# Performance work log

Measured on AMD Instinct MI355X. Metric: run time of the kernel, lower is better.

Reference implementation:

```python
import jax, jax.numpy as jnp
import numpy as np

NUM_USERS = 100000
NUM_ITEMS = 50000
N_NODES = NUM_USERS + NUM_ITEMS
N_EDGES = 2_000_000
D = 64          # embedding_dim
HEADS = 4
F1 = D // HEADS  # per-head out dim of gat1
BATCH = 16384
NEG_SLOPE = 0.2  # PyG GATConv default negative_slope


def setup_inputs() -> dict:
    key = jax.random.key(0)
    ks = jax.random.split(key, 13)
    inp = {}
    inp["edge_index"] = jax.random.randint(ks[0], (2, N_EDGES), 0, N_NODES, dtype=jnp.int64)
    inp["batch_user_idx"] = jax.random.randint(ks[1], (BATCH,), 0, NUM_USERS, dtype=jnp.int64)
    inp["batch_item_idx"] = jax.random.randint(ks[2], (BATCH,), 0, NUM_ITEMS, dtype=jnp.int64)
    # Embedding tables (nn.init.normal_ std=0.01)
    inp["user_emb"] = 0.01 * jax.random.normal(ks[3], (NUM_USERS, D), dtype=jnp.float32)
    inp["item_emb"] = 0.01 * jax.random.normal(ks[4], (NUM_ITEMS, D), dtype=jnp.float32)
    # gat1: GATConv(64, 16, heads=4, concat=True)
    inp["W1"] = jax.random.normal(ks[5], (D, HEADS * F1), dtype=jnp.float32) / np.sqrt(D)
    inp["a_src1"] = jax.random.normal(ks[6], (HEADS, F1), dtype=jnp.float32) / np.sqrt(F1)
    inp["a_dst1"] = jax.random.normal(ks[7], (HEADS, F1), dtype=jnp.float32) / np.sqrt(F1)
    inp["b1"] = jnp.zeros((HEADS * F1,), dtype=jnp.float32)
    # gat2: GATConv(64, 64, heads=1)
    inp["W2"] = jax.random.normal(ks[8], (D, D), dtype=jnp.float32) / np.sqrt(D)
    inp["a_src2"] = jax.random.normal(ks[9], (1, D), dtype=jnp.float32) / np.sqrt(D)
    inp["a_dst2"] = jax.random.normal(ks[10], (1, D), dtype=jnp.float32) / np.sqrt(D)
    inp["b2"] = jnp.zeros((D,), dtype=jnp.float32)
    return inp


def _gat_conv(x, src, dst, W, a_src, a_dst, b, num_nodes):
    """PyG GATConv (eval mode, concat, self-loops already in src/dst)."""
    H, F = a_src.shape
    h = (x @ W).reshape(num_nodes, H, F)                 # [N,H,F]
    alpha_s = jnp.einsum('nhf,hf->nh', h, a_src)         # [N,H]
    alpha_d = jnp.einsum('nhf,hf->nh', h, a_dst)
    e = alpha_s[src] + alpha_d[dst]                      # [E,H]
    e = jax.nn.leaky_relu(e, NEG_SLOPE)
    # scatter-softmax over destination neighborhoods
    m = jax.ops.segment_max(e, dst, num_segments=num_nodes)   # [N,H]
    e = jnp.exp(e - m[dst])
    denom = jax.ops.segment_sum(e, dst, num_segments=num_nodes)
    alpha = e / denom[dst]                               # [E,H]
    msg = h[src] * alpha[:, :, None]                     # [E,H,F]
    agg = jax.ops.segment_sum(msg, dst, num_segments=num_nodes)  # [N,H,F]
    return agg.reshape(num_nodes, H * F) + b


def reference(user_emb, item_emb, W1, a_src1, a_dst1, b1,
              W2, a_src2, a_dst2, b2,
              edge_index, batch_user_idx, batch_item_idx):
    x = jnp.concatenate([user_emb, item_emb], axis=0)    # [N,D]
    n = x.shape[0]
    loop = jnp.arange(n, dtype=edge_index.dtype)          # add_self_loops=True
    src = jnp.concatenate([edge_index[0], loop])
    dst = jnp.concatenate([edge_index[1], loop])
    x = jax.nn.elu(_gat_conv(x, src, dst, W1, a_src1, a_dst1, b1, n))
    x = jax.nn.elu(_gat_conv(x, src, dst, W2, a_src2, a_dst2, b2, n))
    u = x[batch_user_idx]
    v = x[batch_item_idx + NUM_USERS]
    return jax.nn.sigmoid(jnp.sum(u * v, axis=1))        # [BATCH]
```

## Files before the change

kernel.cpp:

```cpp
#include <hip/hip_runtime.h>
#include <math.h>

#define SHIFT 8
#define NBMAX 1024
#define CAP   4096
#define TILE  8192
#define HSCALE 64.0f

typedef float v2f __attribute__((ext_vector_type(2)));
typedef short bf16x8 __attribute__((ext_vector_type(8)));
typedef float f32x4 __attribute__((ext_vector_type(4)));

__device__ __forceinline__ unsigned short f2bf(float f) {
    unsigned u = __float_as_uint(f);
    unsigned r = u + 0x7FFFu + ((u >> 16) & 1u);
    return (unsigned short)(r >> 16);
}
__device__ __forceinline__ unsigned pack2bf(float lo, float hi) {
    return (unsigned)f2bf(lo) | ((unsigned)f2bf(hi) << 16);
}
__device__ __forceinline__ float bflo(unsigned u) { return __uint_as_float(u << 16); }
__device__ __forceinline__ float bfhi(unsigned u) { return __uint_as_float(u & 0xFFFF0000u); }


__global__ void k_prep_w(const float* __restrict__ W1, const float* __restrict__ W2,
                         unsigned short* __restrict__ WT1, unsigned short* __restrict__ WT2,
                         unsigned* __restrict__ gcur, int NB) {
    int t = blockIdx.x * 256 + threadIdx.x;
    if (t < 4096) {
        int n = t & 63, k = t >> 6;
        WT1[n * 64 + k] = f2bf(W1[k * 64 + n]);
        WT2[n * 64 + k] = f2bf(W2[k * 64 + n]);
    }
    if (t < NB) gcur[t] = (unsigned)t * CAP;
}


__global__ __launch_bounds__(512) void k_partition(
    const int* __restrict__ src, const int* __restrict__ dst, int E,
    unsigned* __restrict__ gcur, unsigned* __restrict__ pairs, int NB) {
    __shared__ unsigned lh[NBMAX];
    __shared__ unsigned lcur[NBMAX];
    int t = threadIdx.x;
    for (int q = t; q < NB; q += 512) lh[q] = 0;
    __syncthreads();
    int base = blockIdx.x * TILE;
    int end = min(E, base + TILE);
    for (int i = base + t; i < end; i += 512)
        atomicAdd(&lh[((unsigned)dst[i]) >> SHIFT], 1u);
    __syncthreads();
    for (int q = t; q < NB; q += 512) {
        unsigned c = lh[q];
        lcur[q] = c ? atomicAdd(&gcur[q], c) : 0u;
    }
    __syncthreads();
    for (int i = base + t; i < end; i += 512) {
        unsigned d = (unsigned)dst[i];
        unsigned pos = atomicAdd(&lcur[d >> SHIFT], 1u);
        pairs[pos] = ((d & 255u) << 18) | (unsigned)src[i];
    }
}

__global__ __launch_bounds__(512) void k_bucket_sort(
    const unsigned* __restrict__ pairs, const unsigned* __restrict__ gcur,
    unsigned* __restrict__ beg, unsigned* __restrict__ endd,
    int* __restrict__ srt, int N, int NB) {
    __shared__ unsigned lh[256];
    __shared__ unsigned lcur[256];
    __shared__ unsigned sh[256];
    __shared__ int ssrt[CAP];
    int b = blockIdx.x;
    int t = threadIdx.x;
    unsigned s0 = (unsigned)b * CAP;
    int cnt = (int)(gcur[b] - s0);
    if (t < 256) lh[t] = 0;
    __syncthreads();
    for (int i = t; i < cnt; i += 512)
        atomicAdd(&lh[pairs[s0 + i] >> 18], 1u);
    __syncthreads();
    unsigned deg_t = 0;
    if (t < 256) { deg_t = lh[t]; sh[t] = deg_t; }
    __syncthreads();
    for (int off = 1; off < 256; off <<= 1) {
        unsigned x = 0;
        if (t < 256 && t >= off) x = sh[t - off];
        __syncthreads();
        if (t < 256) sh[t] += x;
        __syncthreads();
    }
    if (t < 256) {
        unsigned excl = sh[t] - deg_t;
        lcur[t] = excl;
        int node = (b << SHIFT) + t;
        if (node < N) { beg[node] = s0 + excl; endd[node] = s0 + excl + deg_t; }
    }
    __syncthreads();
    for (int i = t; i < cnt; i += 512) {
        unsigned pk = pairs[s0 + i];
        unsigned p = atomicAdd(&lcur[pk >> 18], 1u);
        ssrt[p] = (int)(pk & 0x3FFFFu);
    }
    __syncthreads();
    for (int i = t; i < cnt; i += 512) srt[s0 + i] = ssrt[i];
}


template <int HT, int BIN>
__global__ __launch_bounds__(256) void k_linear_mfma(
    const void* __restrict__ xav, const void* __restrict__ xbv, int split,
    const unsigned short* __restrict__ WTg,
    const float* __restrict__ a_src, const float* __restrict__ a_dst,
    unsigned char* __restrict__ h, float* __restrict__ as_out,
    float* __restrict__ ad_out, int N) {
    __shared__ unsigned short sX[64 * 72];
    __shared__ unsigned short sWT[64 * 72];
    __shared__ float sH[64 * 68];
    int t = threadIdx.x;
    int nodeBase = blockIdx.x * 64;

    {
        int r = t >> 2, c4 = (t & 3) * 16;
        int n = nodeBase + r;
        uint4 A = {0,0,0,0}, Bv = {0,0,0,0};
        if (BIN) {
            if (n < N) {
                const unsigned short* row = (const unsigned short*)xav + (size_t)n * 64 + c4;
                A  = ((const uint4*)(const void*)row)[0];
                Bv = ((const uint4*)(const void*)row)[1];
            }
        } else {
            float4 v0 = {0,0,0,0}, v1 = {0,0,0,0}, v2 = {0,0,0,0}, v3 = {0,0,0,0};
            if (n < N) {
                const float* row = (n < split) ? ((const float*)xav + (size_t)n * 64 + c4)
                                               : ((const float*)xbv + (size_t)(n - split) * 64 + c4);
                const float4* r4 = (const float4*)row;
                v0 = r4[0]; v1 = r4[1]; v2 = r4[2]; v3 = r4[3];
            }
            A  = make_uint4(pack2bf(v0.x, v0.y), pack2bf(v0.z, v0.w),
                            pack2bf(v1.x, v1.y), pack2bf(v1.z, v1.w));
            Bv = make_uint4(pack2bf(v2.x, v2.y), pack2bf(v2.z, v2.w),
                            pack2bf(v3.x, v3.y), pack2bf(v3.z, v3.w));
        }
        *(uint4*)(void*)(sX + r * 72 + c4) = A;
        *(uint4*)(void*)(sX + r * 72 + c4 + 8) = Bv;
        const uint4* wsrc = (const uint4*)(const void*)WTg;
        int base = (r * 64 + c4) >> 3;
        *(uint4*)(void*)(sWT + r * 72 + c4) = wsrc[base];
        *(uint4*)(void*)(sWT + r * 72 + c4 + 8) = wsrc[base + 1];
    }
    __syncthreads();

    {
        int lane = t & 63, w = t >> 6;
        int gl = lane & 15, quad = lane >> 4;
        int m0 = w * 16;
        const bf16x8 a0 = *(const bf16x8*)(void*)(sX + (m0 + gl) * 72 + quad * 8);
        const bf16x8 a1 = *(const bf16x8*)(void*)(sX + (m0 + gl) * 72 + 32 + quad * 8);
        f32x4 acc[4];
#pragma unroll
        for (int tt = 0; tt < 4; ++tt) {
            const bf16x8 b0 = *(const bf16x8*)(void*)(sWT + (tt * 16 + gl) * 72 + quad * 8);
            const bf16x8 b1 = *(const bf16x8*)(void*)(sWT + (tt * 16 + gl) * 72 + 32 + quad * 8);
            f32x4 c = {0.f, 0.f, 0.f, 0.f};
            c = __builtin_amdgcn_mfma_f32_16x16x32_bf16(a0, b0, c, 0, 0, 0);
            c = __builtin_amdgcn_mfma_f32_16x16x32_bf16(a1, b1, c, 0, 0, 0);
            acc[tt] = c;
        }
#pragma unroll
        for (int tt = 0; tt < 4; ++tt)
#pragma unroll
            for (int rr = 0; rr < 4; ++rr)
                sH[(m0 + quad * 4 + rr) * 68 + tt * 16 + gl] = acc[tt][rr];
    }
    __syncthreads();

    {
        int m = t >> 2, p = t & 3;
        int n = nodeBase + m;
        const float4* sp = (const float4*)(void*)(sH + m * 68 + p * 16);
        float4 q0 = sp[0], q1 = sp[1], q2 = sp[2], q3 = sp[3];
        float hv[16] = {q0.x,q0.y,q0.z,q0.w, q1.x,q1.y,q1.z,q1.w,
                        q2.x,q2.y,q2.z,q2.w, q3.x,q3.y,q3.z,q3.w};
        if (n < N) {
            unsigned dwords[4];
#pragma unroll
            for (int q = 0; q < 4; ++q) {
                int d0 = __builtin_amdgcn_cvt_pk_fp8_f32(hv[4*q] * HSCALE, hv[4*q+1] * HSCALE, 0, false);
                d0 = __builtin_amdgcn_cvt_pk_fp8_f32(hv[4*q+2] * HSCALE, hv[4*q+3] * HSCALE, d0, true);
                dwords[q] = (unsigned)d0;
            }
            ((uint4*)h)[(size_t)n * 4 + p] = make_uint4(dwords[0], dwords[1], dwords[2], dwords[3]);
            float ps = 0.f, pd = 0.f;
#pragma unroll
            for (int i = 0; i < 16; ++i) {
                ps = fmaf(hv[i], a_src[p * 16 + i], ps);
                pd = fmaf(hv[i], a_dst[p * 16 + i], pd);
            }
            if (HT == 4) {
                as_out[n * 4 + p] = ps;
                ad_out[n * 4 + p] = pd;
            } else {
                ps += __shfl_xor(ps, 1, 64); ps += __shfl_xor(ps, 2, 64);
                pd += __shfl_xor(pd, 1, 64); pd += __shfl_xor(pd, 2, 64);
                if (p == 0) { as_out[n] = ps; ad_out[n] = pd; }
            }
        }
    }
}

template <int HT>
__global__ __launch_bounds__(256, 4) void k_gat(
                      const int* __restrict__ srt, const unsigned* __restrict__ beg,
                      const unsigned* __restrict__ endd,
                      const unsigned* __restrict__ hq, const float* __restrict__ as,
                      const float* __restrict__ ad, const float* __restrict__ b,
                      unsigned* __restrict__ xout, int N) {
    __shared__ unsigned s_vo[4][4][40];
    __shared__ float    s_w[4][4][(HT == 4) ? 164 : 40];

    int t = threadIdx.x;
    int lane = t & 63;
    int wv = t >> 6;
    int gl = lane & 15;
    int g  = lane >> 4;
    int wid = (int)((blockIdx.x * blockDim.x + t) >> 6);
    int d = wid * 4 + g;
    bool active = d < N;
    const int hh = (HT == 4) ? (gl >> 2) : 0;
    const unsigned gl4 = (unsigned)gl << 2;
    const char* hqb = (const char*)hq;
    const char* asb = (const char*)as;

    float adv = 0.f, l = 0.f;
    float a0 = 0.f, a1 = 0.f, a2 = 0.f, a3 = 0.f;
    int kb = 0, end = 0;
    if (active) {
        adv = ad[d * HT + hh];
        float e0 = as[d * HT + hh] + adv;
        e0 = (e0 > 0.f) ? e0 : 0.2f * e0;
        float w0 = __expf(e0);
        unsigned dw = hq[(size_t)d * 16 + gl];
        v2f lo = __builtin_amdgcn_cvt_pk_f32_fp8((int)dw, false);
        v2f hi = __builtin_amdgcn_cvt_pk_f32_fp8((int)dw, true);
        l = w0;
        a0 = w0 * lo.x; a1 = w0 * lo.y; a2 = w0 * hi.x; a3 = w0 * hi.y;
        kb = (int)beg[d];
        end = (int)endd[d];
    }

    int m = end - kb;
    while (__ballot(m > 0)) {
        unsigned v0 = 0, v1 = 0;
        if (gl < m)      v0 = ((unsigned)srt[kb + gl]) << 6;
        if (gl + 16 < m) v1 = ((unsigned)srt[kb + gl + 16]) << 6;

        if (HT == 1) {
            float as0 = 0.f, as1 = 0.f;
            if (gl < m)      as0 = *(const float*)(asb + (v0 >> 4));
            if (gl + 16 < m) as1 = *(const float*)(asb + (v1 >> 4));
            s_vo[wv][g][gl]      = v0;
            s_vo[wv][g][gl + 16] = v1;
            asm volatile("s_waitcnt lgkmcnt(0)" ::: "memory");
            __builtin_amdgcn_sched_barrier(0);
            unsigned rr[32];
            const uint4* vob = (const uint4*)(const void*)&s_vo[wv][g][0];
#pragma unroll
            for (int c = 0; c < 8; ++c) {
                uint4 vv = vob[c];
                rr[4*c+0] = *(const unsigned*)(hqb + (vv.x + gl4));
                rr[4*c+1] = *(const unsigned*)(hqb + (vv.y + gl4));
                rr[4*c+2] = *(const unsigned*)(hqb + (vv.z + gl4));
                rr[4*c+3] = *(const unsigned*)(hqb + (vv.w + gl4));
            }
            float w0 = 0.f, w1 = 0.f;
            if (gl < m) {
                float e = as0 + adv;
                e = (e > 0.f) ? e : 0.2f * e;
                w0 = __expf(e);
            }
            if (gl + 16 < m) {
                float e = as1 + adv;
                e = (e > 0.f) ? e : 0.2f * e;
                w1 = __expf(e);
            }
            float wsum = w0 + w1;
            wsum += __shfl_xor(wsum, 1, 64);
            wsum += __shfl_xor(wsum, 2, 64);
            wsum += __shfl_xor(wsum, 4, 64);
            wsum += __shfl_xor(wsum, 8, 64);
            l += wsum;
            s_w[wv][g][gl]      = w0;
            s_w[wv][g][gl + 16] = w1;
            asm volatile("s_waitcnt lgkmcnt(0)" ::: "memory");
            __builtin_amdgcn_sched_barrier(0);
            const float4* wrd = (const float4*)(const void*)&s_w[wv][g][0];
#pragma unroll
            for (int c = 0; c < 8; ++c) {
                float4 wc = wrd[c];
                float wj[4] = {wc.x, wc.y, wc.z, wc.w};
#pragma unroll
                for (int j = 0; j < 4; ++j) {
                    float w = wj[j];
                    unsigned rv = rr[4*c + j];
                    v2f lo = __builtin_amdgcn_cvt_pk_f32_fp8((int)rv, false);
                    v2f hi = __builtin_amdgcn_cvt_pk_f32_fp8((int)rv, true);
                    a0 = fmaf(w, lo.x, a0);
                    a1 = fmaf(w, lo.y, a1);
                    a2 = fmaf(w, hi.x, a2);
                    a3 = fmaf(w, hi.y, a3);
                }
            }
        } else {
            s_vo[wv][g][gl]      = v0;
            s_vo[wv][g][gl + 16] = v1;
            asm volatile("s_waitcnt lgkmcnt(0)" ::: "memory");
            __builtin_amdgcn_sched_barrier(0);
            int eb = (gl & 3) << 3;
            const uint4* vop = (const uint4*)(const void*)&s_vo[wv][g][eb];
            uint4 va = vop[0], vb = vop[1];
            unsigned vs[8] = {va.x, va.y, va.z, va.w, vb.x, vb.y, vb.z, vb.w};
            float av[8];
#pragma unroll
            for (int r = 0; r < 8; ++r)
                av[r] = *(const float*)(asb + ((vs[r] >> 2) + ((unsigned)hh << 2)));
            unsigned rr[32];
            const uint4* vob = (const uint4*)(const void*)&s_vo[wv][g][0];
#pragma unroll
            for (int c = 0; c < 8; ++c) {
                uint4 vv = vob[c];
                rr[4*c+0] = *(const unsigned*)(hqb + (vv.x + gl4));
                rr[4*c+1] = *(const unsigned*)(hqb + (vv.y + gl4));
                rr[4*c+2] = *(const unsigned*)(hqb + (vv.z + gl4));
                rr[4*c+3] = *(const unsigned*)(hqb + (vv.w + gl4));
            }
            float wq[8];
#pragma unroll
            for (int r = 0; r < 8; ++r) {
                wq[r] = 0.f;
                if (eb + r < m) {
                    float e = av[r] + adv;
                    e = (e > 0.f) ? e : 0.2f * e;
                    wq[r] = __expf(e);
                }
            }
            float wsum = ((wq[0] + wq[1]) + (wq[2] + wq[3]))
                       + ((wq[4] + wq[5]) + (wq[6] + wq[7]));
            wsum += __shfl_xor(wsum, 1, 64);
            wsum += __shfl_xor(wsum, 2, 64);
            l += wsum;
            float4* wp = (float4*)(void*)&s_w[wv][g][hh * 40 + eb];
            wp[0] = make_float4(wq[0], wq[1], wq[2], wq[3]);
            wp[1] = make_float4(wq[4], wq[5], wq[6], wq[7]);
            asm volatile("s_waitcnt lgkmcnt(0)" ::: "memory");
            __builtin_amdgcn_sched_barrier(0);
            const float4* wrd = (const float4*)(const void*)&s_w[wv][g][hh * 40];
#pragma unroll
            for (int c = 0; c < 8; ++c) {
                float4 wc = wrd[c];
                float wj[4] = {wc.x, wc.y, wc.z, wc.w};
#pragma unroll
                for (int j = 0; j < 4; ++j) {
                    float w = wj[j];
                    unsigned rv = rr[4*c + j];
                    v2f lo = __builtin_amdgcn_cvt_pk_f32_fp8((int)rv, false);
                    v2f hi = __builtin_amdgcn_cvt_pk_f32_fp8((int)rv, true);
                    a0 = fmaf(w, lo.x, a0);
                    a1 = fmaf(w, lo.y, a1);
                    a2 = fmaf(w, hi.x, a2);
                    a3 = fmaf(w, hi.y, a3);
                }
            }
        }
        kb += 32;
        m = end - kb;
    }

    if (active) {
        float4 bb4 = ((const float4*)b)[gl];
        float rs = 1.f / (l * HSCALE);
        float v0 = a0 * rs + bb4.x;
        float v1 = a1 * rs + bb4.y;
        float v2 = a2 * rs + bb4.z;
        float v3 = a3 * rs + bb4.w;
        float o0 = (v0 > 0.f) ? v0 : expm1f(v0);
        float o1 = (v1 > 0.f) ? v1 : expm1f(v1);
        float o2 = (v2 > 0.f) ? v2 : expm1f(v2);
        float o3 = (v3 > 0.f) ? v3 : expm1f(v3);
        ((uint2*)xout)[(size_t)d * 16 + gl] = make_uint2(pack2bf(o0, o1), pack2bf(o2, o3));
    }
}

__global__ void k_dot_sig(const uint2* __restrict__ x2, const int* __restrict__ uidx,
                          const int* __restrict__ vidx, float* __restrict__ out,
                          int batch, int numUsers) {
    int lane = threadIdx.x & 63;
    int gl = lane & 15;
    int q = (int)(((blockIdx.x * blockDim.x + threadIdx.x) >> 6) * 4 + (lane >> 4));
    if (q >= batch) return;
    int u = uidx[q];
    int v = vidx[q] + numUsers;
    uint2 a = x2[(size_t)u * 16 + gl];
    uint2 c = x2[(size_t)v * 16 + gl];
    float p = bflo(a.x) * bflo(c.x) + bfhi(a.x) * bfhi(c.x)
            + bflo(a.y) * bflo(c.y) + bfhi(a.y) * bfhi(c.y);
#pragma unroll
    for (int off = 1; off < 16; off <<= 1) p += __shfl_xor(p, off, 64);
    if (gl == 0) out[q] = 1.f / (1.f + __expf(-p));
}


static inline int cdiv(long long a, long long b) { return (int)((a + b - 1) / b); }

extern "C" void kernel_launch(void* const* d_in, const int* in_sizes, int n_in,
                              void* d_out, int out_size, void* d_ws, size_t ws_size,
                              hipStream_t stream) {
    const int* edge_index = (const int*)d_in[0];
    const int* buidx      = (const int*)d_in[1];
    const int* biidx      = (const int*)d_in[2];
    const float* user_emb = (const float*)d_in[3];
    const float* item_emb = (const float*)d_in[4];
    const float* W1     = (const float*)d_in[5];
    const float* a_src1 = (const float*)d_in[6];
    const float* a_dst1 = (const float*)d_in[7];
    const float* b1     = (const float*)d_in[8];
    const float* W2     = (const float*)d_in[9];
    const float* a_src2 = (const float*)d_in[10];
    const float* a_dst2 = (const float*)d_in[11];
    const float* b2     = (const float*)d_in[12];
    float* out = (float*)d_out;

    const int E  = in_sizes[0] / 2;
    const int B  = in_sizes[1];
    const int NU = in_sizes[3] / 64;
    const int NI = in_sizes[4] / 64;
    const int N  = NU + NI;
    const int NB = cdiv(N, 1 << SHIFT);

    const int* src = edge_index;
    const int* dst = edge_index + E;

    float* ws = (float*)d_ws;
    size_t off = 0;
    unsigned* x_buf  = (unsigned*)(ws + off); off += (size_t)N * 32;
    unsigned* h_buf  = (unsigned*)(ws + off); off += (size_t)N * 16;
    float*    as_b   = ws + off; off += (size_t)N * 4;
    float*    ad_b   = ws + off; off += (size_t)N * 4;
    unsigned* gcur_b = (unsigned*)(ws + off); off += NBMAX;
    unsigned* beg_b  = (unsigned*)(ws + off); off += (size_t)N;
    unsigned* end_b  = (unsigned*)(ws + off); off += (size_t)N;
    unsigned* pairs_b= (unsigned*)(ws + off); off += (size_t)NB * CAP;
    int*      srt_b  = (int*)(ws + off); off += (size_t)NB * CAP;
    unsigned short* wt1_b = (unsigned short*)(ws + off); off += 2048;
    unsigned short* wt2_b = (unsigned short*)(ws + off); off += 2048;

    const int BS = 256;

    k_prep_w<<<16, BS, 0, stream>>>(W1, W2, wt1_b, wt2_b, gcur_b, NB);
    k_partition<<<cdiv(E, TILE), 512, 0, stream>>>(src, dst, E, gcur_b, pairs_b, NB);
    k_bucket_sort<<<NB, 512, 0, stream>>>(pairs_b, gcur_b, beg_b, end_b, srt_b, N, NB);

    k_linear_mfma<4, 0><<<cdiv(N, 64), BS, 0, stream>>>(user_emb, item_emb, NU, wt1_b,
                                                        a_src1, a_dst1,
                                                        (unsigned char*)h_buf, as_b, ad_b, N);
    k_gat<4><<<cdiv((long long)N * 16, BS), BS, 0, stream>>>(
        srt_b, beg_b, end_b, h_buf, as_b, ad_b, b1, x_buf, N);

    k_linear_mfma<1, 1><<<cdiv(N, 64), BS, 0, stream>>>(x_buf, x_buf, N, wt2_b,
                                                        a_src2, a_dst2,
                                                        (unsigned char*)h_buf, as_b, ad_b, N);
    k_gat<1><<<cdiv((long long)N * 16, BS), BS, 0, stream>>>(
        srt_b, beg_b, end_b, h_buf, as_b, ad_b, b2, x_buf, N);

    k_dot_sig<<<cdiv((long long)B * 16, BS), BS, 0, stream>>>(
        (const uint2*)x_buf, buidx, biidx, out, B, NU);
}
```

Baseline: 250.9 us.

## Skip second half of gather chunk when wave degrees small; fold weight prep into partition

The GAT aggregation loop now takes the maximum remaining degree across each wave's four destinations and skips the second 16-neighbor half of each 32-edge chunk (index loads, feature gathers, FMAs) when no destination needs it. Accumulators switch to packed float2 vectors so the compiler can emit packed FMA instructions. The k_prep_w kernel is removed: weight transposition moves into k_partition, and the bucket cursor init becomes a memset with bucket offsets added inside partition. This trims one launch and wasted work for low-degree nodes (average degree is about 14), at the cost of extra shuffles and branches per iteration.

```diff
diff --git a/kernel.cpp b/kernel.cpp
--- a/kernel.cpp
+++ b/kernel.cpp
@@ -23,25 +23,22 @@
 __device__ __forceinline__ float bfhi(unsigned u) { return __uint_as_float(u & 0xFFFF0000u); }
 
 
-__global__ void k_prep_w(const float* __restrict__ W1, const float* __restrict__ W2,
-                         unsigned short* __restrict__ WT1, unsigned short* __restrict__ WT2,
-                         unsigned* __restrict__ gcur, int NB) {
-    int t = blockIdx.x * 256 + threadIdx.x;
-    if (t < 4096) {
-        int n = t & 63, k = t >> 6;
-        WT1[n * 64 + k] = f2bf(W1[k * 64 + n]);
-        WT2[n * 64 + k] = f2bf(W2[k * 64 + n]);
-    }
-    if (t < NB) gcur[t] = (unsigned)t * CAP;
-}
-
-
 __global__ __launch_bounds__(512) void k_partition(
     const int* __restrict__ src, const int* __restrict__ dst, int E,
-    unsigned* __restrict__ gcur, unsigned* __restrict__ pairs, int NB) {
+    unsigned* __restrict__ gcur, unsigned* __restrict__ pairs, int NB,
+    const float* __restrict__ W1, const float* __restrict__ W2,
+    unsigned short* __restrict__ WT1, unsigned short* __restrict__ WT2) {
     __shared__ unsigned lh[NBMAX];
     __shared__ unsigned lcur[NBMAX];
     int t = threadIdx.x;
+    {
+        int gt = blockIdx.x * 512 + t;
+        if (gt < 4096) {
+            int n = gt & 63, k = gt >> 6;
+            WT1[n * 64 + k] = f2bf(W1[k * 64 + n]);
+            WT2[n * 64 + k] = f2bf(W2[k * 64 + n]);
+        }
+    }
     for (int q = t; q < NB; q += 512) lh[q] = 0;
     __syncthreads();
     int base = blockIdx.x * TILE;
@@ -51,7 +48,7 @@
     __syncthreads();
     for (int q = t; q < NB; q += 512) {
         unsigned c = lh[q];
-        lcur[q] = c ? atomicAdd(&gcur[q], c) : 0u;
+        lcur[q] = c ? ((unsigned)q * CAP + atomicAdd(&gcur[q], c)) : 0u;
     }
     __syncthreads();
     for (int i = base + t; i < end; i += 512) {
@@ -72,7 +69,7 @@
     int b = blockIdx.x;
     int t = threadIdx.x;
     unsigned s0 = (unsigned)b * CAP;
-    int cnt = (int)(gcur[b] - s0);
+    int cnt = (int)gcur[b];
     if (t < 256) lh[t] = 0;
     __syncthreads();
     for (int i = t; i < cnt; i += 512)
@@ -232,7 +229,7 @@
     const char* asb = (const char*)as;
 
     float adv = 0.f, l = 0.f;
-    float a0 = 0.f, a1 = 0.f, a2 = 0.f, a3 = 0.f;
+    v2f acc01 = {0.f, 0.f}, acc23 = {0.f, 0.f};
     int kb = 0, end = 0;
     if (active) {
         adv = ad[d * HT + hh];
@@ -243,42 +240,58 @@
         v2f lo = __builtin_amdgcn_cvt_pk_f32_fp8((int)dw, false);
         v2f hi = __builtin_amdgcn_cvt_pk_f32_fp8((int)dw, true);
         l = w0;
-        a0 = w0 * lo.x; a1 = w0 * lo.y; a2 = w0 * hi.x; a3 = w0 * hi.y;
+        v2f wv2 = {w0, w0};
+        acc01 = wv2 * lo;
+        acc23 = wv2 * hi;
         kb = (int)beg[d];
         end = (int)endd[d];
     }
 
     int m = end - kb;
     while (__ballot(m > 0)) {
+        int mm = max(m, __shfl_xor(m, 16, 64));
+        mm = max(mm, __shfl_xor(mm, 32, 64));
+        const bool up = mm > 16;
+
         unsigned v0 = 0, v1 = 0;
-        if (gl < m)      v0 = ((unsigned)srt[kb + gl]) << 6;
-        if (gl + 16 < m) v1 = ((unsigned)srt[kb + gl + 16]) << 6;
+        if (gl < m)            v0 = ((unsigned)srt[kb + gl]) << 6;
+        if (up && gl + 16 < m) v1 = ((unsigned)srt[kb + gl + 16]) << 6;
 
         if (HT == 1) {
             float as0 = 0.f, as1 = 0.f;
-            if (gl < m)      as0 = *(const float*)(asb + (v0 >> 4));
-            if (gl + 16 < m) as1 = *(const float*)(asb + (v1 >> 4));
-            s_vo[wv][g][gl]      = v0;
-            s_vo[wv][g][gl + 16] = v1;
+            if (gl < m)            as0 = *(const float*)(asb + (v0 >> 4));
+            if (up && gl + 16 < m) as1 = *(const float*)(asb + (v1 >> 4));
+            s_vo[wv][g][gl] = v0;
+            if (up) s_vo[wv][g][gl + 16] = v1;
             asm volatile("s_waitcnt lgkmcnt(0)" ::: "memory");
             __builtin_amdgcn_sched_barrier(0);
             unsigned rr[32];
             const uint4* vob = (const uint4*)(const void*)&s_vo[wv][g][0];
 #pragma unroll
-            for (int c = 0; c < 8; ++c) {
+            for (int c = 0; c < 4; ++c) {
                 uint4 vv = vob[c];
                 rr[4*c+0] = *(const unsigned*)(hqb + (vv.x + gl4));
                 rr[4*c+1] = *(const unsigned*)(hqb + (vv.y + gl4));
                 rr[4*c+2] = *(const unsigned*)(hqb + (vv.z + gl4));
                 rr[4*c+3] = *(const unsigned*)(hqb + (vv.w + gl4));
             }
+            if (up) {
+#pragma unroll
+                for (int c = 4; c < 8; ++c) {
+                    uint4 vv = vob[c];
+                    rr[4*c+0] = *(const unsigned*)(hqb + (vv.x + gl4));
+                    rr[4*c+1] = *(const unsigned*)(hqb + (vv.y + gl4));
+                    rr[4*c+2] = *(const unsigned*)(hqb + (vv.z + gl4));
+                    rr[4*c+3] = *(const unsigned*)(hqb + (vv.w + gl4));
+                }
+            }
             float w0 = 0.f, w1 = 0.f;
             if (gl < m) {
                 float e = as0 + adv;
                 e = (e > 0.f) ? e : 0.2f * e;
                 w0 = __expf(e);
             }
-            if (gl + 16 < m) {
+            if (up && gl + 16 < m) {
                 float e = as1 + adv;
                 e = (e > 0.f) ? e : 0.2f * e;
                 w1 = __expf(e);
@@ -289,13 +302,13 @@
             wsum += __shfl_xor(wsum, 4, 64);
             wsum += __shfl_xor(wsum, 8, 64);
             l += wsum;
-            s_w[wv][g][gl]      = w0;
-            s_w[wv][g][gl + 16] = w1;
+            s_w[wv][g][gl] = w0;
+            if (up) s_w[wv][g][gl + 16] = w1;
             asm volatile("s_waitcnt lgkmcnt(0)" ::: "memory");
             __builtin_amdgcn_sched_barrier(0);
             const float4* wrd = (const float4*)(const void*)&s_w[wv][g][0];
 #pragma unroll
-            for (int c = 0; c < 8; ++c) {
+            for (int c = 0; c < 4; ++c) {
                 float4 wc = wrd[c];
                 float wj[4] = {wc.x, wc.y, wc.z, wc.w};
 #pragma unroll
@@ -304,15 +317,31 @@
                     unsigned rv = rr[4*c + j];
                     v2f lo = __builtin_amdgcn_cvt_pk_f32_fp8((int)rv, false);
                     v2f hi = __builtin_amdgcn_cvt_pk_f32_fp8((int)rv, true);
-                    a0 = fmaf(w, lo.x, a0);
-                    a1 = fmaf(w, lo.y, a1);
-                    a2 = fmaf(w, hi.x, a2);
-                    a3 = fmaf(w, hi.y, a3);
+                    v2f wv2 = {w, w};
+                    acc01 += wv2 * lo;
+                    acc23 += wv2 * hi;
+                }
+            }
+            if (up) {
+#pragma unroll
+                for (int c = 4; c < 8; ++c) {
+                    float4 wc = wrd[c];
+                    float wj[4] = {wc.x, wc.y, wc.z, wc.w};
+#pragma unroll
+                    for (int j = 0; j < 4; ++j) {
+                        float w = wj[j];
+                        unsigned rv = rr[4*c + j];
+                        v2f lo = __builtin_amdgcn_cvt_pk_f32_fp8((int)rv, false);
+                        v2f hi = __builtin_amdgcn_cvt_pk_f32_fp8((int)rv, true);
+                        v2f wv2 = {w, w};
+                        acc01 += wv2 * lo;
+                        acc23 += wv2 * hi;
+                    }
                 }
             }
         } else {
             s_vo[wv][g][gl]      = v0;
-            s_vo[wv][g][gl + 16] = v1;
+            s_vo[wv][g][gl + 16] = (up && gl + 16 < m) ? v1 : 0u;
             asm volatile("s_waitcnt lgkmcnt(0)" ::: "memory");
             __builtin_amdgcn_sched_barrier(0);
             int eb = (gl & 3) << 3;
@@ -326,12 +355,22 @@
             unsigned rr[32];
             const uint4* vob = (const uint4*)(const void*)&s_vo[wv][g][0];
 #pragma unroll
-            for (int c = 0; c < 8; ++c) {
+            for (int c = 0; c < 4; ++c) {
                 uint4 vv = vob[c];
                 rr[4*c+0] = *(const unsigned*)(hqb + (vv.x + gl4));
                 rr[4*c+1] = *(const unsigned*)(hqb + (vv.y + gl4));
                 rr[4*c+2] = *(const unsigned*)(hqb + (vv.z + gl4));
                 rr[4*c+3] = *(const unsigned*)(hqb + (vv.w + gl4));
+            }
+            if (up) {
+#pragma unroll
+                for (int c = 4; c < 8; ++c) {
+                    uint4 vv = vob[c];
+                    rr[4*c+0] = *(const unsigned*)(hqb + (vv.x + gl4));
+                    rr[4*c+1] = *(const unsigned*)(hqb + (vv.y + gl4));
+                    rr[4*c+2] = *(const unsigned*)(hqb + (vv.z + gl4));
+                    rr[4*c+3] = *(const unsigned*)(hqb + (vv.w + gl4));
+                }
             }
             float wq[8];
 #pragma unroll
@@ -355,7 +394,7 @@
             __builtin_amdgcn_sched_barrier(0);
             const float4* wrd = (const float4*)(const void*)&s_w[wv][g][hh * 40];
 #pragma unroll
-            for (int c = 0; c < 8; ++c) {
+            for (int c = 0; c < 4; ++c) {
                 float4 wc = wrd[c];
                 float wj[4] = {wc.x, wc.y, wc.z, wc.w};
 #pragma unroll
@@ -364,10 +403,26 @@
                     unsigned rv = rr[4*c + j];
                     v2f lo = __builtin_amdgcn_cvt_pk_f32_fp8((int)rv, false);
                     v2f hi = __builtin_amdgcn_cvt_pk_f32_fp8((int)rv, true);
-                    a0 = fmaf(w, lo.x, a0);
-                    a1 = fmaf(w, lo.y, a1);
-                    a2 = fmaf(w, hi.x, a2);
-                    a3 = fmaf(w, hi.y, a3);
+                    v2f wv2 = {w, w};
+                    acc01 += wv2 * lo;
+                    acc23 += wv2 * hi;
+                }
+            }
+            if (up) {
+#pragma unroll
+                for (int c = 4; c < 8; ++c) {
+                    float4 wc = wrd[c];
+                    float wj[4] = {wc.x, wc.y, wc.z, wc.w};
+#pragma unroll
+                    for (int j = 0; j < 4; ++j) {
+                        float w = wj[j];
+                        unsigned rv = rr[4*c + j];
+                        v2f lo = __builtin_amdgcn_cvt_pk_f32_fp8((int)rv, false);
+                        v2f hi = __builtin_amdgcn_cvt_pk_f32_fp8((int)rv, true);
+                        v2f wv2 = {w, w};
+                        acc01 += wv2 * lo;
+                        acc23 += wv2 * hi;
+                    }
                 }
             }
         }
@@ -378,10 +433,10 @@
     if (active) {
         float4 bb4 = ((const float4*)b)[gl];
         float rs = 1.f / (l * HSCALE);
-        float v0 = a0 * rs + bb4.x;
-        float v1 = a1 * rs + bb4.y;
-        float v2 = a2 * rs + bb4.z;
-        float v3 = a3 * rs + bb4.w;
+        float v0 = acc01.x * rs + bb4.x;
+        float v1 = acc01.y * rs + bb4.y;
+        float v2 = acc23.x * rs + bb4.z;
+        float v3 = acc23.y * rs + bb4.w;
         float o0 = (v0 > 0.f) ? v0 : expm1f(v0);
         float o1 = (v1 > 0.f) ? v1 : expm1f(v1);
         float o2 = (v2 > 0.f) ? v2 : expm1f(v2);
@@ -455,8 +510,9 @@
 
     const int BS = 256;
 
-    k_prep_w<<<16, BS, 0, stream>>>(W1, W2, wt1_b, wt2_b, gcur_b, NB);
-    k_partition<<<cdiv(E, TILE), 512, 0, stream>>>(src, dst, E, gcur_b, pairs_b, NB);
+    hipMemsetAsync(gcur_b, 0, NBMAX * sizeof(unsigned), stream);
+    k_partition<<<cdiv(E, TILE), 512, 0, stream>>>(src, dst, E, gcur_b, pairs_b, NB,
+                                                   W1, W2, wt1_b, wt2_b);
     k_bucket_sort<<<NB, 512, 0, stream>>>(pairs_b, gcur_b, beg_b, end_b, srt_b, N, NB);
 
     k_linear_mfma<4, 0><<<cdiv(N, 64), BS, 0, stream>>>(user_emb, item_emb, NU, wt1_b,
```

Measured after the change: 252.6 us. About the same (+0.7%).

## Merge bucket sort and first linear layer into one launch; fold weight prep into partition

Applied to the files above, without the earlier changes.

Weight transposition to bf16 moves into the partition kernel, and the per-bucket cursor init becomes a memset, with offsets now relative to each bucket base. The bucket sort and the layer-1 MFMA linear transform become one kernel: the first NB blocks sort and the rest compute h, sharing LDS through a union. The aim is to remove launch overhead and let two independent stages run concurrently on the GPU. The cost is that the linear blocks now use 512 threads with half of them idle in the MFMA and epilogue phases, and the union raises LDS per block to the larger of the two layouts.

```diff
diff --git a/kernel.cpp b/kernel.cpp
--- a/kernel.cpp
+++ b/kernel.cpp
@@ -23,25 +23,22 @@
 __device__ __forceinline__ float bfhi(unsigned u) { return __uint_as_float(u & 0xFFFF0000u); }
 
 
-__global__ void k_prep_w(const float* __restrict__ W1, const float* __restrict__ W2,
-                         unsigned short* __restrict__ WT1, unsigned short* __restrict__ WT2,
-                         unsigned* __restrict__ gcur, int NB) {
-    int t = blockIdx.x * 256 + threadIdx.x;
-    if (t < 4096) {
-        int n = t & 63, k = t >> 6;
-        WT1[n * 64 + k] = f2bf(W1[k * 64 + n]);
-        WT2[n * 64 + k] = f2bf(W2[k * 64 + n]);
-    }
-    if (t < NB) gcur[t] = (unsigned)t * CAP;
-}
-
-
 __global__ __launch_bounds__(512) void k_partition(
     const int* __restrict__ src, const int* __restrict__ dst, int E,
-    unsigned* __restrict__ gcur, unsigned* __restrict__ pairs, int NB) {
+    unsigned* __restrict__ gcur, unsigned* __restrict__ pairs, int NB,
+    const float* __restrict__ W1, const float* __restrict__ W2,
+    unsigned short* __restrict__ WT1, unsigned short* __restrict__ WT2) {
     __shared__ unsigned lh[NBMAX];
     __shared__ unsigned lcur[NBMAX];
     int t = threadIdx.x;
+    {
+        int gt = blockIdx.x * 512 + t;
+        if (gt < 4096) {
+            int n = gt & 63, k = gt >> 6;
+            WT1[n * 64 + k] = f2bf(W1[k * 64 + n]);
+            WT2[n * 64 + k] = f2bf(W2[k * 64 + n]);
+        }
+    }
     for (int q = t; q < NB; q += 512) lh[q] = 0;
     __syncthreads();
     int base = blockIdx.x * TILE;
@@ -51,7 +48,7 @@
     __syncthreads();
     for (int q = t; q < NB; q += 512) {
         unsigned c = lh[q];
-        lcur[q] = c ? atomicAdd(&gcur[q], c) : 0u;
+        lcur[q] = c ? ((unsigned)q * CAP + atomicAdd(&gcur[q], c)) : 0u;
     }
     __syncthreads();
     for (int i = base + t; i < end; i += 512) {
@@ -61,47 +58,125 @@
     }
 }
 
-__global__ __launch_bounds__(512) void k_bucket_sort(
+__global__ __launch_bounds__(512) void k_buck_lin(
     const unsigned* __restrict__ pairs, const unsigned* __restrict__ gcur,
     unsigned* __restrict__ beg, unsigned* __restrict__ endd,
-    int* __restrict__ srt, int N, int NB) {
-    __shared__ unsigned lh[256];
-    __shared__ unsigned lcur[256];
-    __shared__ unsigned sh[256];
-    __shared__ int ssrt[CAP];
-    int b = blockIdx.x;
+    int* __restrict__ srt, int N, int NB,
+    const float* __restrict__ xa, const float* __restrict__ xb, int split,
+    const unsigned short* __restrict__ WTg,
+    const float* __restrict__ a_src, const float* __restrict__ a_dst,
+    unsigned char* __restrict__ h, float* __restrict__ as_out,
+    float* __restrict__ ad_out) {
+    __shared__ union U {
+        struct { unsigned lh[256]; unsigned lcur[256]; unsigned sh[256]; int ssrt[CAP]; } b;
+        struct { unsigned short sX[64 * 72]; unsigned short sWT[64 * 72]; float sH[64 * 68]; } l;
+    } u;
     int t = threadIdx.x;
-    unsigned s0 = (unsigned)b * CAP;
-    int cnt = (int)(gcur[b] - s0);
-    if (t < 256) lh[t] = 0;
-    __syncthreads();
-    for (int i = t; i < cnt; i += 512)
-        atomicAdd(&lh[pairs[s0 + i] >> 18], 1u);
-    __syncthreads();
-    unsigned deg_t = 0;
-    if (t < 256) { deg_t = lh[t]; sh[t] = deg_t; }
-    __syncthreads();
-    for (int off = 1; off < 256; off <<= 1) {
-        unsigned x = 0;
-        if (t < 256 && t >= off) x = sh[t - off];
-        __syncthreads();
-        if (t < 256) sh[t] += x;
-        __syncthreads();
-    }
-    if (t < 256) {
-        unsigned excl = sh[t] - deg_t;
-        lcur[t] = excl;
-        int node = (b << SHIFT) + t;
-        if (node < N) { beg[node] = s0 + excl; endd[node] = s0 + excl + deg_t; }
-    }
-    __syncthreads();
-    for (int i = t; i < cnt; i += 512) {
-        unsigned pk = pairs[s0 + i];
-        unsigned p = atomicAdd(&lcur[pk >> 18], 1u);
-        ssrt[p] = (int)(pk & 0x3FFFFu);
-    }
-    __syncthreads();
-    for (int i = t; i < cnt; i += 512) srt[s0 + i] = ssrt[i];
+
+    if ((int)blockIdx.x < NB) {
+        int b = blockIdx.x;
+        unsigned s0 = (unsigned)b * CAP;
+        int cnt = (int)gcur[b];
+        if (t < 256) u.b.lh[t] = 0;
+        __syncthreads();
+        for (int i = t; i < cnt; i += 512)
+            atomicAdd(&u.b.lh[pairs[s0 + i] >> 18], 1u);
+        __syncthreads();
+        unsigned deg_t = 0;
+        if (t < 256) { deg_t = u.b.lh[t]; u.b.sh[t] = deg_t; }
+        __syncthreads();
+        for (int off = 1; off < 256; off <<= 1) {
+            unsigned x = 0;
+            if (t < 256 && t >= off) x = u.b.sh[t - off];
+            __syncthreads();
+            if (t < 256) u.b.sh[t] += x;
+            __syncthreads();
+        }
+        if (t < 256) {
+            unsigned excl = u.b.sh[t] - deg_t;
+            u.b.lcur[t] = excl;
+            int node = (b << SHIFT) + t;
+            if (node < N) { beg[node] = s0 + excl; endd[node] = s0 + excl + deg_t; }
+        }
+        __syncthreads();
+        for (int i = t; i < cnt; i += 512) {
+            unsigned pk = pairs[s0 + i];
+            unsigned p = atomicAdd(&u.b.lcur[pk >> 18], 1u);
+            u.b.ssrt[p] = (int)(pk & 0x3FFFFu);
+        }
+        __syncthreads();
+        for (int i = t; i < cnt; i += 512) srt[s0 + i] = u.b.ssrt[i];
+    } else {
+        int nodeBase = ((int)blockIdx.x - NB) * 64;
+        {
+            int r = t >> 3, c8 = (t & 7) * 8;
+            int n = nodeBase + r;
+            float4 v0 = {0,0,0,0}, v1 = {0,0,0,0};
+            if (n < N) {
+                const float* row = (n < split) ? (xa + (size_t)n * 64 + c8)
+                                               : (xb + (size_t)(n - split) * 64 + c8);
+                const float4* r4 = (const float4*)row;
+                v0 = r4[0]; v1 = r4[1];
+            }
+            uint4 A = make_uint4(pack2bf(v0.x, v0.y), pack2bf(v0.z, v0.w),
+                                 pack2bf(v1.x, v1.y), pack2bf(v1.z, v1.w));
+            *(uint4*)(void*)(u.l.sX + r * 72 + c8) = A;
+            const uint4* wsrc = (const uint4*)(const void*)WTg;
+            *(uint4*)(void*)(u.l.sWT + r * 72 + c8) = wsrc[r * 8 + (c8 >> 3)];
+        }
+        __syncthreads();
+        {
+            int lane = t & 63, w = t >> 6;
+            if (w < 4) {
+                int gl = lane & 15, quad = lane >> 4;
+                int m0 = w * 16;
+                const bf16x8 a0 = *(const bf16x8*)(void*)(u.l.sX + (m0 + gl) * 72 + quad * 8);
+                const bf16x8 a1 = *(const bf16x8*)(void*)(u.l.sX + (m0 + gl) * 72 + 32 + quad * 8);
+                f32x4 acc[4];
+#pragma unroll
+                for (int tt = 0; tt < 4; ++tt) {
+                    const bf16x8 b0 = *(const bf16x8*)(void*)(u.l.sWT + (tt * 16 + gl) * 72 + quad * 8);
+                    const bf16x8 b1 = *(const bf16x8*)(void*)(u.l.sWT + (tt * 16 + gl) * 72 + 32 + quad * 8);
+                    f32x4 c = {0.f, 0.f, 0.f, 0.f};
+                    c = __builtin_amdgcn_mfma_f32_16x16x32_bf16(a0, b0, c, 0, 0, 0);
+                    c = __builtin_amdgcn_mfma_f32_16x16x32_bf16(a1, b1, c, 0, 0, 0);
+                    acc[tt] = c;
+                }
+#pragma unroll
+                for (int tt = 0; tt < 4; ++tt)
+#pragma unroll
+                    for (int rr = 0; rr < 4; ++rr)
+                        u.l.sH[(m0 + quad * 4 + rr) * 68 + tt * 16 + gl] = acc[tt][rr];
+            }
+        }
+        __syncthreads();
+        if (t < 256) {
+            int m = t >> 2, p = t & 3;
+            int n = nodeBase + m;
+            const float4* sp = (const float4*)(void*)(u.l.sH + m * 68 + p * 16);
+            float4 q0 = sp[0], q1 = sp[1], q2 = sp[2], q3 = sp[3];
+            float hv[16] = {q0.x,q0.y,q0.z,q0.w, q1.x,q1.y,q1.z,q1.w,
+                            q2.x,q2.y,q2.z,q2.w, q3.x,q3.y,q3.z,q3.w};
+            if (n < N) {
+                unsigned dwords[4];
+#pragma unroll
+                for (int q = 0; q < 4; ++q) {
+                    int d0 = __builtin_amdgcn_cvt_pk_fp8_f32(hv[4*q] * HSCALE, hv[4*q+1] * HSCALE, 0, false);
+                    d0 = __builtin_amdgcn_cvt_pk_fp8_f32(hv[4*q+2] * HSCALE, hv[4*q+3] * HSCALE, d0, true);
+                    dwords[q] = (unsigned)d0;
+                }
+                ((uint4*)h)[(size_t)n * 4 + p] = make_uint4(dwords[0], dwords[1], dwords[2], dwords[3]);
+                float ps = 0.f, pd = 0.f;
+#pragma unroll
+                for (int i = 0; i < 16; ++i) {
+                    ps = fmaf(hv[i], a_src[p * 16 + i], ps);
+                    pd = fmaf(hv[i], a_dst[p * 16 + i], pd);
+                }
+                as_out[n * 4 + p] = ps;
+                ad_out[n * 4 + p] = pd;
+            }
+        }
+    }
 }
 
 
@@ -455,13 +530,15 @@
 
     const int BS = 256;
 
-    k_prep_w<<<16, BS, 0, stream>>>(W1, W2, wt1_b, wt2_b, gcur_b, NB);
-    k_partition<<<cdiv(E, TILE), 512, 0, stream>>>(src, dst, E, gcur_b, pairs_b, NB);
-    k_bucket_sort<<<NB, 512, 0, stream>>>(pairs_b, gcur_b, beg_b, end_b, srt_b, N, NB);
-
-    k_linear_mfma<4, 0><<<cdiv(N, 64), BS, 0, stream>>>(user_emb, item_emb, NU, wt1_b,
-                                                        a_src1, a_dst1,
-                                                        (unsigned char*)h_buf, as_b, ad_b, N);
+    hipMemsetAsync(gcur_b, 0, NBMAX * sizeof(unsigned), stream);
+    k_partition<<<cdiv(E, TILE), 512, 0, stream>>>(src, dst, E, gcur_b, pairs_b, NB,
+                                                   W1, W2, wt1_b, wt2_b);
+
+    k_buck_lin<<<NB + cdiv(N, 64), 512, 0, stream>>>(
+        pairs_b, gcur_b, beg_b, end_b, srt_b, N, NB,
+        user_emb, item_emb, NU, wt1_b, a_src1, a_dst1,
+        (unsigned char*)h_buf, as_b, ad_b);
+
     k_gat<4><<<cdiv((long long)N * 16, BS), BS, 0, stream>>>(
         srt_b, beg_b, end_b, h_buf, as_b, ad_b, b1, x_buf, N);
 
```

Result: no change. 248.8 us (-0.9%).
